# Kernel tuning notes

Measured on AMD Instinct MI355X. Metric: run time of the kernel, lower is better.

Reference implementation:

```python
import jax, jax.numpy as jnp
import numpy as np

T, B, H, W, C = 256, 1024, 9, 9, 3
CTX, HID, ACT = 64, 256, 7

def setup_inputs() -> dict:
    key = jax.random.key(0)
    ks = jax.random.split(key, 16)
    s = 0.05
    return {
        'image': jax.random.normal(ks[0], (T, B, H, W, C), jnp.float32),
        'agent_dir': jax.random.randint(ks[1], (T, B), 0, 4, jnp.int32),
        'dones': jax.random.bernoulli(ks[2], 0.02, (T, B)),
        'context': jax.random.normal(ks[3], (B, CTX), jnp.float32),
        'c0': jnp.zeros((B, HID), jnp.float32),
        'h0': jnp.zeros((B, HID), jnp.float32),
        'conv_k': jax.random.normal(ks[4], (3, 3, C, 16), jnp.float32) * s,
        'conv_b': jnp.zeros((16,), jnp.float32),
        'emb_k': jax.random.normal(ks[5], (4, 5), jnp.float32) * s,
        'emb_b': jnp.zeros((5,), jnp.float32),
        'wi': jax.random.normal(ks[6], (784 + 5 + CTX, 4 * HID), jnp.float32) * s,
        'wh': jax.random.normal(ks[7], (HID, 4 * HID), jnp.float32) * s,
        'b_lstm': jnp.zeros((4 * HID,), jnp.float32),
        'a0_k': jax.random.normal(ks[8], (HID, 32), jnp.float32) * s,
        'a0_b': jnp.zeros((32,), jnp.float32),
        'a1_k': jax.random.normal(ks[9], (32, ACT), jnp.float32) * s,
        'a1_b': jnp.zeros((ACT,), jnp.float32),
        'cr0_k': jax.random.normal(ks[10], (HID, 32), jnp.float32) * s,
        'cr0_b': jnp.zeros((32,), jnp.float32),
        'cr1_k': jax.random.normal(ks[11], (32, 1), jnp.float32) * s,
        'cr1_b': jnp.zeros((1,), jnp.float32),
    }


def reference(image, agent_dir, dones, context, c0, h0, conv_k, conv_b,
              emb_k, emb_b, wi, wh, b_lstm, a0_k, a0_b, a1_k, a1_b,
              cr0_k, cr0_b, cr1_k, cr1_b):
    t, b = image.shape[:2]
    # Conv(16, 3x3, VALID) over flattened (T*B) batch, NHWC
    x = image.reshape(t * b, *image.shape[2:])
    img = jax.lax.conv_general_dilated(
        x, conv_k, window_strides=(1, 1), padding='VALID',
        dimension_numbers=('NHWC', 'HWIO', 'NHWC')) + conv_b
    img = jax.nn.relu(img.reshape(t, b, -1))  # (T, B, 784)
    # direction embedding: one_hot(4) -> Dense(5)
    dir_e = jax.nn.one_hot(agent_dir, 4, dtype=img.dtype) @ emb_k + emb_b
    # context broadcast over time
    ctx = jnp.broadcast_to(context[None], (t, b, context.shape[-1]))
    emb = jnp.concatenate([img, dir_e, ctx], axis=-1)  # (T, B, 853)
    # precompute input-side LSTM gates (big batched GEMM outside the scan)
    xg = emb @ wi + b_lstm  # (T, B, 4*HID)

    def step(carry, inp):
        c, h = carry
        xg_t, done = inp
        mask = done[:, None]
        c = jnp.where(mask, c0, c)  # reset carry at episode boundaries
        h = jnp.where(mask, h0, h)
        gates = xg_t + h @ wh
        i, f, g, o = jnp.split(gates, 4, axis=-1)  # flax order: i, f, g, o
        new_c = jax.nn.sigmoid(f) * c + jax.nn.sigmoid(i) * jnp.tanh(g)
        new_h = jax.nn.sigmoid(o) * jnp.tanh(new_c)
        return (new_c, new_h), new_h

    (c_fin, h_fin), ys = jax.lax.scan(step, (c0, h0), (xg, dones))
    actor = jax.nn.relu(ys @ a0_k + a0_b)
    logits = actor @ a1_k + a1_b  # Categorical logits
    critic = jax.nn.relu(ys @ cr0_k + cr0_b)
    value = jnp.squeeze(critic @ cr1_k + cr1_b, axis=-1)
    return c_fin, h_fin, logits, value
```

## Files before the change

### kernel.cpp

```cpp
#include <hip/hip_runtime.h>
#include <hip/hip_fp8.h>

typedef __bf16 bf16;
typedef __bf16 bf16x8 __attribute__((ext_vector_type(8)));
typedef __bf16 bf16x4 __attribute__((ext_vector_type(4)));
typedef float  f32x4  __attribute__((ext_vector_type(4)));

#define T_DIM 256
#define B_DIM 1024
#define HID   256
#define G4    1024
#define KIMG  784
#define KPAD  800
#define KEXT  864
#define CTXD  64
#define MROWS (T_DIM*B_DIM)
#define WPITCH 264

__device__ __forceinline__ void gll16(const void* g, void* l) {
  __builtin_amdgcn_global_load_lds((const __attribute__((address_space(1))) void*)g,
                                   (__attribute__((address_space(3))) void*)l, 16, 0, 0);
}
__device__ __forceinline__ float sigm(float x) { return 1.f / (1.f + __expf(-x)); }
__device__ __forceinline__ float tanh_(float x) {
  x = fminf(fmaxf(x, -15.f), 15.f);
  float e = __expf(2.f * x);
  return (e - 1.f) / (e + 1.f);
}
__device__ __forceinline__ void bar_lds() {
  asm volatile("s_waitcnt lgkmcnt(0)\n\ts_barrier" ::: "memory");
}
__device__ __forceinline__ unsigned char to_fp8(float f) {
  __hip_fp8_e4m3 v(f);
  return *reinterpret_cast<unsigned char*>(&v);
}

__global__ void k_wiT(const float* __restrict__ wi, bf16* __restrict__ wiT) {
  int n = blockIdx.x;
  for (int k = threadIdx.x; k < KEXT; k += 256) {
    float v = 0.f;
    if (k < KIMG) v = wi[(long)k * G4 + n];
    else if (k >= 800) v = wi[(long)(k - 11) * G4 + n];
    wiT[(long)n * KEXT + k] = (bf16)v;
  }
}
__global__ void k_ext(const float* __restrict__ ctx, bf16* __restrict__ ext) {
  int idx = blockIdx.x * 256 + threadIdx.x;
  ext[idx] = (bf16)ctx[idx];
}
__global__ void k_wh8(const float* __restrict__ wh, unsigned char* __restrict__ wh8) {
  int n = blockIdx.x;
  int k = threadIdx.x;
#pragma unroll
  for (int g = 0; g < 4; ++g)
    wh8[g * 65536 + n * 256 + k] = to_fp8(wh[k * G4 + g * 256 + n]);
}
__global__ void k_W0T(const float* __restrict__ a0k, const float* __restrict__ cr0k,
                      bf16* __restrict__ w0t) {
  int n = blockIdx.x;
  int k = threadIdx.x;
  float v = (n < 32) ? a0k[k * 32 + n] : cr0k[k * 32 + (n - 32)];
  w0t[n * HID + k] = (bf16)v;
}
__global__ void k_dirgate(const float* __restrict__ wi, const float* __restrict__ emb_k,
                          const float* __restrict__ emb_b, const float* __restrict__ b_lstm,
                          float* __restrict__ dir_gate) {
  int d = blockIdx.x;
  for (int n = threadIdx.x; n < G4; n += 256) {
    float s = b_lstm[n];
#pragma unroll
    for (int j = 0; j < 5; ++j) s += (emb_k[d * 5 + j] + emb_b[j]) * wi[(KIMG + j) * G4 + n];
    dir_gate[d * G4 + n] = s;
  }
}

#define CONV_ROWS 8
__global__ void k_conv(const float* __restrict__ img, const float* __restrict__ ck,
                       const float* __restrict__ cb, bf16* __restrict__ out) {
  __shared__ float s_img[CONV_ROWS * 243];
  __shared__ float s_k[432];
  __shared__ float s_b[16];
  long r0 = (long)blockIdx.x * CONV_ROWS;
  const float* src = img + r0 * 243;
  for (int i = threadIdx.x; i < CONV_ROWS * 243; i += 256) s_img[i] = src[i];
  for (int i = threadIdx.x; i < 432; i += 256) s_k[i] = ck[i];
  if (threadIdx.x < 16) s_b[threadIdx.x] = cb[threadIdx.x];
  __syncthreads();
  for (int idx = threadIdx.x; idx < CONV_ROWS * KPAD; idx += 256) {
    int r = idx / KPAD, c = idx % KPAD;
    float v = 0.f;
    if (c < KIMG) {
      int pix = c >> 4, ch = c & 15;
      int oy = pix / 7, ox = pix % 7;
      const float* ib = s_img + r * 243 + (oy * 9 + ox) * 3;
      v = s_b[ch];
#pragma unroll
      for (int ky = 0; ky < 3; ++ky)
#pragma unroll
        for (int kx = 0; kx < 3; ++kx)
#pragma unroll
          for (int cc = 0; cc < 3; ++cc)
            v += ib[(ky * 9 + kx) * 3 + cc] * s_k[((ky * 3 + kx) * 3 + cc) * 16 + ch];
      v = fmaxf(v, 0.f);
    }
    out[r0 * KPAD + idx] = (bf16)v;
  }
}

__global__ __launch_bounds__(256, 2)
void k_gemm_xg(const bf16* __restrict__ A, const bf16* __restrict__ ext,
               const bf16* __restrict__ Bt, const float* __restrict__ dir_gate,
               const int* __restrict__ agent_dir, bf16* __restrict__ xg) {
  __shared__ __align__(16) bf16 As[128 * 32];
  __shared__ __align__(16) bf16 Bs[128 * 32];
  const int bid = blockIdx.x;
  const int xcd = bid & 7, local = bid >> 3;
  const long m0 = (long)(xcd * 256 + (local >> 3)) * 128;
  const int n0 = (local & 7) * 128;
  const int tid = threadIdx.x, wave = tid >> 6, lane = tid & 63;
  const int row16 = lane & 15, k8 = (lane >> 4) * 8, rowg = (lane >> 4) * 4;
  const int wr = (wave >> 1) * 64, wc = (wave & 1) * 64;

  const bf16* a_src0 = A + (m0 + tid / 4) * KPAD + (tid % 4) * 8;
  const bf16* a_src1 = A + (m0 + 64 + tid / 4) * KPAD + (tid % 4) * 8;
  const bf16* e_src0 = ext + (long)(((m0) & 1023) + tid / 4) * CTXD + (tid % 4) * 8;
  const bf16* e_src1 = ext + (long)(((m0 + 64) & 1023) + tid / 4) * CTXD + (tid % 4) * 8;
  const bf16* b_src0 = Bt + (long)(n0 + tid / 4) * KEXT + (tid % 4) * 8;
  const bf16* b_src1 = Bt + (long)(n0 + 64 + tid / 4) * KEXT + (tid % 4) * 8;
  bf16* asd0 = As + wave * 512;
  bf16* asd1 = As + 2048 + wave * 512;
  bf16* bsd0 = Bs + wave * 512;
  bf16* bsd1 = Bs + 2048 + wave * 512;

  f32x4 acc[4][4];
  const f32x4 zero = {0.f, 0.f, 0.f, 0.f};
#pragma unroll
  for (int i = 0; i < 4; ++i)
#pragma unroll
    for (int j = 0; j < 4; ++j) acc[i][j] = zero;

  for (int ks = 0; ks < 27; ++ks) {
    if (ks < 25) {
      const int ko = ks * 32;
      gll16(a_src0 + ko, asd0);
      gll16(a_src1 + ko, asd1);
    } else {
      const int ko = (ks - 25) * 32;
      gll16(e_src0 + ko, asd0);
      gll16(e_src1 + ko, asd1);
    }
    const int kb = ks * 32;
    gll16(b_src0 + kb, bsd0);
    gll16(b_src1 + kb, bsd1);
    __syncthreads();
    bf16x8 af[4], bfr[4];
#pragma unroll
    for (int i = 0; i < 4; ++i)
      af[i] = *(const bf16x8*)(As + (wr + 16 * i + row16) * 32 + k8);
#pragma unroll
    for (int j = 0; j < 4; ++j)
      bfr[j] = *(const bf16x8*)(Bs + (wc + 16 * j + row16) * 32 + k8);
#pragma unroll
    for (int i = 0; i < 4; ++i)
#pragma unroll
      for (int j = 0; j < 4; ++j)
        acc[i][j] = __builtin_amdgcn_mfma_f32_16x16x32_bf16(af[i], bfr[j], acc[i][j], 0, 0, 0);
    __syncthreads();
  }
#pragma unroll
  for (int i = 0; i < 4; ++i)
#pragma unroll
    for (int j = 0; j < 4; ++j)
#pragma unroll
      for (int r = 0; r < 4; ++r) {
        long row = m0 + wr + 16 * i + rowg + r;
        int colj = n0 + wc + 16 * j + row16;
        int dv = agent_dir[row];
        float base = dir_gate[dv * G4 + colj];
        int u = colj & 255, g = colj >> 8;
        xg[row * G4 + u * 4 + g] = (bf16)(acc[i][j][r] + base);
      }
}

__global__ __launch_bounds__(1024)
void k_lstm(const bf16* __restrict__ xg, const unsigned char* __restrict__ wh8,
            const int* __restrict__ dones,
            const float* __restrict__ c0, const float* __restrict__ h0,
            bf16* __restrict__ ys, float* __restrict__ cfin, float* __restrict__ hfin) {
  __shared__ __align__(16) unsigned char wi8_lds[256 * WPITCH];
  __shared__ __align__(16) unsigned char wg8_lds[256 * WPITCH];
  __shared__ __align__(16) unsigned char h8_lds[16 * WPITCH];
  const int tid = threadIdx.x;
  const int w = tid >> 6, lane = tid & 63;
  const int col = lane & 15;
  const int kq = lane >> 4;
  const int k8 = kq * 8;
  const int rowg = kq * 4;
  const int b0 = blockIdx.x * 16;
  const int ju = 16 * w + col;

  for (int i = tid; i < 256 * 32; i += 1024) {
    int row = i >> 5, c = i & 31;
    *(long long*)(wi8_lds + row * WPITCH + c * 8) =
        *(const long long*)(wh8 + row * 256 + c * 8);
    *(long long*)(wg8_lds + row * WPITCH + c * 8) =
        *(const long long*)(wh8 + 2 * 65536 + row * 256 + c * 8);
  }
  for (int i = tid; i < 16 * HID; i += 1024) {
    int m = i >> 8, j = i & 255;
    h8_lds[m * WPITCH + j] = to_fp8(h0[(b0 + m) * HID + j]);
  }

  float creg[4], c0reg[4];
  unsigned char h0b8[4];
#pragma unroll
  for (int r = 0; r < 4; ++r) {
    float v = c0[(b0 + rowg + r) * HID + ju];
    creg[r] = v; c0reg[r] = v;
    h0b8[r] = to_fp8(h0[(b0 + rowg + r) * HID + ju]);
  }
  const unsigned char* wfp = wh8 + 1 * 65536 + ju * 256 + k8;
  const unsigned char* wop = wh8 + 3 * 65536 + ju * 256 + k8;

  int4 dnA = *(const int4*)(dones + b0 + rowg);
  bf16x4 xc[4];
  {
    const bf16* xb = xg + (long)(b0 + rowg) * G4 + ju * 4;
#pragma unroll
    for (int r = 0; r < 4; ++r)
      xc[r] = *(const bf16x4*)(xb + (long)r * G4);
  }
  long long bf_cur, bf_nxt, bo_cur, bo_nxt;
  bf_cur = *(const long long*)(wfp);
  bo_cur = *(const long long*)(wop);
  __syncthreads();

#pragma unroll 1
  for (int t = 0; t < T_DIM; ++t) {
    const int tn = (t + 1 < T_DIM) ? t + 1 : (T_DIM - 1);
    f32x4 acc[4];
    const f32x4 zero = {0.f, 0.f, 0.f, 0.f};
#pragma unroll
    for (int g = 0; g < 4; ++g) acc[g] = zero;

    int4 dnB;
#pragma unroll
    for (int ks = 0; ks < 8; ++ks) {
      {
        const int kn = (ks + 1) & 7;
        bf_nxt = *(const long long*)(wfp + kn * 32);
        bo_nxt = *(const long long*)(wop + kn * 32);
      }
      long long a8 = *(const long long*)(h8_lds + col * WPITCH + ks * 32 + k8);
      long long bi8 = *(const long long*)(wi8_lds + ju * WPITCH + ks * 32 + k8);
      long long bg8 = *(const long long*)(wg8_lds + ju * WPITCH + ks * 32 + k8);
      acc[0] = __builtin_amdgcn_mfma_f32_16x16x32_fp8_fp8(a8, bi8, acc[0], 0, 0, 0);
      acc[1] = __builtin_amdgcn_mfma_f32_16x16x32_fp8_fp8(a8, bf_cur, acc[1], 0, 0, 0);
      acc[2] = __builtin_amdgcn_mfma_f32_16x16x32_fp8_fp8(a8, bg8, acc[2], 0, 0, 0);
      acc[3] = __builtin_amdgcn_mfma_f32_16x16x32_fp8_fp8(a8, bo_cur, acc[3], 0, 0, 0);
      bf_cur = bf_nxt; bo_cur = bo_nxt;
      if (ks == 2)
        dnB = *(const int4*)(dones + (long)tn * B_DIM + b0 + rowg);
    }
    bar_lds();

    int dc[4] = {dnA.x, dnA.y, dnA.z, dnA.w};
    int dx[4] = {dnB.x, dnB.y, dnB.z, dnB.w};
#pragma unroll
    for (int r = 0; r < 4; ++r) {
      float c_old = dc[r] ? c0reg[r] : creg[r];
      float gi = acc[0][r] + (float)xc[r][0];
      float gf = acc[1][r] + (float)xc[r][1];
      float gg = acc[2][r] + (float)xc[r][2];
      float go = acc[3][r] + (float)xc[r][3];
      float cn = sigm(gf) * c_old + sigm(gi) * tanh_(gg);
      float hn = sigm(go) * tanh_(cn);
      creg[r] = cn;
      int m = rowg + r;
      ys[((long)t * B_DIM + b0 + m) * HID + ju] = (bf16)hn;
      h8_lds[m * WPITCH + ju] = dx[r] ? h0b8[r] : to_fp8(hn);
      if (t == T_DIM - 1) {
        cfin[(b0 + m) * HID + ju] = cn;
        hfin[(b0 + m) * HID + ju] = hn;
      }
    }
    {
      const bf16* xb = xg + (long)(tn * B_DIM + b0 + rowg) * G4 + ju * 4;
#pragma unroll
      for (int r = 0; r < 4; ++r)
        xc[r] = *(const bf16x4*)(xb + (long)r * G4);
    }
    dnA = dnB;
    bar_lds();
  }
}

#define H1PITCH 66
__global__ __launch_bounds__(256, 2)
void k_heads(const bf16* __restrict__ ys, const bf16* __restrict__ w0t,
             const float* __restrict__ a0b, const float* __restrict__ cr0b,
             const float* __restrict__ a1k, const float* __restrict__ a1b,
             const float* __restrict__ cr1k, const float* __restrict__ cr1b,
             float* __restrict__ logits, float* __restrict__ value) {
  __shared__ __align__(16) bf16 As[128 * 32];
  __shared__ __align__(16) bf16 Ws[64 * 264];
  __shared__ bf16 h1_lds[128 * H1PITCH];
  __shared__ float w2[32 * 8];
  const int tid = threadIdx.x, wave = tid >> 6, lane = tid & 63;
  const int row16 = lane & 15, k8 = (lane >> 4) * 8, rowg = (lane >> 4) * 4;
  const long m0 = (long)blockIdx.x * 128;
  for (int i = tid; i < 64 * 256; i += 256) {
    int n = i >> 8, k = i & 255;
    Ws[n * 264 + k] = w0t[i];
  }
  if (tid < 224) { int k = tid / 7, c = tid % 7; w2[k * 8 + c] = a1k[tid]; }
  else if (tid < 256) { int k = tid - 224; w2[k * 8 + 7] = cr1k[k]; }
  const bf16* a_src0 = ys + (m0 + tid / 4) * HID + (tid % 4) * 8;
  const bf16* a_src1 = ys + (m0 + 64 + tid / 4) * HID + (tid % 4) * 8;
  bf16* asd0 = As + wave * 512;
  bf16* asd1 = As + 2048 + wave * 512;
  f32x4 acc[2][4];
  const f32x4 zero = {0.f, 0.f, 0.f, 0.f};
#pragma unroll
  for (int i = 0; i < 2; ++i)
#pragma unroll
    for (int j = 0; j < 4; ++j) acc[i][j] = zero;
  for (int ks = 0; ks < 8; ++ks) {
    gll16(a_src0 + ks * 32, asd0);
    gll16(a_src1 + ks * 32, asd1);
    __syncthreads();
    bf16x8 bw[4];
#pragma unroll
    for (int j = 0; j < 4; ++j)
      bw[j] = *(const bf16x8*)(Ws + (16 * j + row16) * 264 + ks * 32 + k8);
#pragma unroll
    for (int i = 0; i < 2; ++i) {
      bf16x8 a = *(const bf16x8*)(As + (32 * wave + 16 * i + row16) * 32 + k8);
#pragma unroll
      for (int j = 0; j < 4; ++j)
        acc[i][j] = __builtin_amdgcn_mfma_f32_16x16x32_bf16(a, bw[j], acc[i][j], 0, 0, 0);
    }
    __syncthreads();
  }
#pragma unroll
  for (int i = 0; i < 2; ++i)
#pragma unroll
    for (int j = 0; j < 4; ++j)
#pragma unroll
      for (int r = 0; r < 4; ++r) {
        int rl = 32 * wave + 16 * i + rowg + r;
        int n = 16 * j + row16;
        float bias = (n < 32) ? a0b[n] : cr0b[n - 32];
        h1_lds[rl * H1PITCH + n] = (bf16)fmaxf(acc[i][j][r] + bias, 0.f);
      }
  __syncthreads();
  if (tid < 128) {
    const bf16* hp = h1_lds + tid * H1PITCH;
    float acc7[7];
#pragma unroll
    for (int c = 0; c < 7; ++c) acc7[c] = a1b[c];
    float accv = cr1b[0];
#pragma unroll 4
    for (int k = 0; k < 32; ++k) {
      float av = (float)hp[k];
      float cv = (float)hp[32 + k];
#pragma unroll
      for (int c = 0; c < 7; ++c) acc7[c] += av * w2[k * 8 + c];
      accv += cv * w2[k * 8 + 7];
    }
    long row = m0 + tid;
#pragma unroll
    for (int c = 0; c < 7; ++c) logits[row * 7 + c] = acc7[c];
    value[row] = accv;
  }
}

extern "C" void kernel_launch(void* const* d_in, const int* in_sizes, int n_in,
                              void* d_out, int out_size, void* d_ws, size_t ws_size,
                              hipStream_t stream) {
  const float* image = (const float*)d_in[0];
  const int* agent_dir = (const int*)d_in[1];
  const int* dones = (const int*)d_in[2];
  const float* context = (const float*)d_in[3];
  const float* c0 = (const float*)d_in[4];
  const float* h0 = (const float*)d_in[5];
  const float* conv_k = (const float*)d_in[6];
  const float* conv_b = (const float*)d_in[7];
  const float* emb_k = (const float*)d_in[8];
  const float* emb_b = (const float*)d_in[9];
  const float* wi = (const float*)d_in[10];
  const float* wh = (const float*)d_in[11];
  const float* b_lstm = (const float*)d_in[12];
  const float* a0_k = (const float*)d_in[13];
  const float* a0_b = (const float*)d_in[14];
  const float* a1_k = (const float*)d_in[15];
  const float* a1_b = (const float*)d_in[16];
  const float* cr0_k = (const float*)d_in[17];
  const float* cr0_b = (const float*)d_in[18];
  const float* cr1_k = (const float*)d_in[19];
  const float* cr1_b = (const float*)d_in[20];

  char* ws = (char*)d_ws;
  const size_t off_conv = 0;
  const size_t off_xg   = 419430400ULL;
  const size_t off_wiT  = off_xg  + 536870912ULL;
  const size_t off_W0T  = off_wiT + 1769472ULL;
  const size_t off_dirg = off_W0T + 32768ULL;
  const size_t off_wh8  = off_dirg + 16384ULL;
  const size_t off_ext  = off_wh8 + 262144ULL;
  const size_t total    = off_ext + 131072ULL;
  if (ws_size < total) return;

  bf16* conv_out = (bf16*)(ws + off_conv);
  bf16* xg       = (bf16*)(ws + off_xg);
  bf16* wiT      = (bf16*)(ws + off_wiT);
  bf16* W0T      = (bf16*)(ws + off_W0T);
  float* dir_gate = (float*)(ws + off_dirg);
  unsigned char* wh8 = (unsigned char*)(ws + off_wh8);
  bf16* ext = (bf16*)(ws + off_ext);
  bf16* ys = (bf16*)(ws + 0);

  float* out_cfin = (float*)d_out;
  float* out_hfin = out_cfin + 262144;
  float* out_logits = out_cfin + 524288;
  float* out_value = out_cfin + 524288 + 1835008;

  k_wiT<<<1024, 256, 0, stream>>>(wi, wiT);
  k_ext<<<256, 256, 0, stream>>>(context, ext);
  k_W0T<<<64, 256, 0, stream>>>(a0_k, cr0_k, W0T);
  k_dirgate<<<4, 256, 0, stream>>>(wi, emb_k, emb_b, b_lstm, dir_gate);
  k_wh8<<<256, 256, 0, stream>>>(wh, wh8);
  k_conv<<<MROWS / CONV_ROWS, 256, 0, stream>>>(image, conv_k, conv_b, conv_out);
  k_gemm_xg<<<16384, 256, 0, stream>>>(conv_out, ext, wiT, dir_gate, agent_dir, xg);
  k_lstm<<<64, 1024, 0, stream>>>(xg, wh8, dones, c0, h0, ys, out_cfin, out_hfin);
  k_heads<<<2048, 256, 0, stream>>>(ys, W0T, a0_b, cr0_b, a1_k, a1_b, cr1_k, cr1_b,
                                    out_logits, out_value);
}
```

Baseline: 2.429 ms.

## Double-buffer LSTM hidden state in LDS and compute conv per pixel

The LSTM recurrence kernel now ping-pongs the fp8 hidden-state buffer between two LDS slots, so one of the two block-wide barriers per timestep can be removed. The conv kernel is also restructured so each thread computes all 16 output channels for one pixel, reusing each input load across channels and writing with vectorized bf16x8 stores. A separate pass zeroes the padded columns. Costs are slightly more LDS and higher register use in the conv kernel.

```diff
diff --git a/kernel.cpp b/kernel.cpp
--- a/kernel.cpp
+++ b/kernel.cpp
@@ -86,24 +86,37 @@
   for (int i = threadIdx.x; i < 432; i += 256) s_k[i] = ck[i];
   if (threadIdx.x < 16) s_b[threadIdx.x] = cb[threadIdx.x];
   __syncthreads();
-  for (int idx = threadIdx.x; idx < CONV_ROWS * KPAD; idx += 256) {
-    int r = idx / KPAD, c = idx % KPAD;
-    float v = 0.f;
-    if (c < KIMG) {
-      int pix = c >> 4, ch = c & 15;
-      int oy = pix / 7, ox = pix % 7;
-      const float* ib = s_img + r * 243 + (oy * 9 + ox) * 3;
-      v = s_b[ch];
-#pragma unroll
-      for (int ky = 0; ky < 3; ++ky)
-#pragma unroll
-        for (int kx = 0; kx < 3; ++kx)
-#pragma unroll
-          for (int cc = 0; cc < 3; ++cc)
-            v += ib[(ky * 9 + kx) * 3 + cc] * s_k[((ky * 3 + kx) * 3 + cc) * 16 + ch];
-      v = fmaxf(v, 0.f);
-    }
-    out[r0 * KPAD + idx] = (bf16)v;
+  if (threadIdx.x < 128) {
+    int r = threadIdx.x >> 4, c = 784 + (threadIdx.x & 15);
+    out[(r0 + r) * KPAD + c] = (bf16)0.f;
+  }
+  for (int pi = threadIdx.x; pi < CONV_ROWS * 49; pi += 256) {
+    int r = pi / 49, p = pi - r * 49;
+    int oy = p / 7, ox = p - oy * 7;
+    const float* ib = s_img + r * 243 + (oy * 9 + ox) * 3;
+    float acc[16];
+#pragma unroll
+    for (int ch = 0; ch < 16; ++ch) acc[ch] = s_b[ch];
+#pragma unroll
+    for (int ky = 0; ky < 3; ++ky)
+#pragma unroll
+      for (int kx = 0; kx < 3; ++kx)
+#pragma unroll
+        for (int cc = 0; cc < 3; ++cc) {
+          float iv = ib[(ky * 9 + kx) * 3 + cc];
+          const float* kp = s_k + ((ky * 3 + kx) * 3 + cc) * 16;
+#pragma unroll
+          for (int ch = 0; ch < 16; ++ch) acc[ch] += iv * kp[ch];
+        }
+    bf16x8 v0, v1;
+#pragma unroll
+    for (int ch = 0; ch < 8; ++ch) {
+      v0[ch] = (bf16)fmaxf(acc[ch], 0.f);
+      v1[ch] = (bf16)fmaxf(acc[ch + 8], 0.f);
+    }
+    bf16* op = out + (r0 + r) * KPAD + p * 16;
+    *(bf16x8*)op = v0;
+    *(bf16x8*)(op + 8) = v1;
   }
 }
 
@@ -189,7 +202,7 @@
             bf16* __restrict__ ys, float* __restrict__ cfin, float* __restrict__ hfin) {
   __shared__ __align__(16) unsigned char wi8_lds[256 * WPITCH];
   __shared__ __align__(16) unsigned char wg8_lds[256 * WPITCH];
-  __shared__ __align__(16) unsigned char h8_lds[16 * WPITCH];
+  __shared__ __align__(16) unsigned char h8_lds[2][16 * WPITCH];
   const int tid = threadIdx.x;
   const int w = tid >> 6, lane = tid & 63;
   const int col = lane & 15;
@@ -208,7 +221,7 @@
   }
   for (int i = tid; i < 16 * HID; i += 1024) {
     int m = i >> 8, j = i & 255;
-    h8_lds[m * WPITCH + j] = to_fp8(h0[(b0 + m) * HID + j]);
+    h8_lds[0][m * WPITCH + j] = to_fp8(h0[(b0 + m) * HID + j]);
   }
 
   float creg[4], c0reg[4];
@@ -234,6 +247,9 @@
   bf_cur = *(const long long*)(wfp);
   bo_cur = *(const long long*)(wop);
   __syncthreads();
+
+  const unsigned char* hr = h8_lds[0];
+  unsigned char* hw = (unsigned char*)h8_lds[1];
 
 #pragma unroll 1
   for (int t = 0; t < T_DIM; ++t) {
@@ -251,7 +267,7 @@
         bf_nxt = *(const long long*)(wfp + kn * 32);
         bo_nxt = *(const long long*)(wop + kn * 32);
       }
-      long long a8 = *(const long long*)(h8_lds + col * WPITCH + ks * 32 + k8);
+      long long a8 = *(const long long*)(hr + col * WPITCH + ks * 32 + k8);
       long long bi8 = *(const long long*)(wi8_lds + ju * WPITCH + ks * 32 + k8);
       long long bg8 = *(const long long*)(wg8_lds + ju * WPITCH + ks * 32 + k8);
       acc[0] = __builtin_amdgcn_mfma_f32_16x16x32_fp8_fp8(a8, bi8, acc[0], 0, 0, 0);
@@ -262,7 +278,6 @@
       if (ks == 2)
         dnB = *(const int4*)(dones + (long)tn * B_DIM + b0 + rowg);
     }
-    bar_lds();
 
     int dc[4] = {dnA.x, dnA.y, dnA.z, dnA.w};
     int dx[4] = {dnB.x, dnB.y, dnB.z, dnB.w};
@@ -278,7 +293,7 @@
       creg[r] = cn;
       int m = rowg + r;
       ys[((long)t * B_DIM + b0 + m) * HID + ju] = (bf16)hn;
-      h8_lds[m * WPITCH + ju] = dx[r] ? h0b8[r] : to_fp8(hn);
+      hw[m * WPITCH + ju] = dx[r] ? h0b8[r] : to_fp8(hn);
       if (t == T_DIM - 1) {
         cfin[(b0 + m) * HID + ju] = cn;
         hfin[(b0 + m) * HID + ju] = hn;
@@ -292,6 +307,7 @@
     }
     dnA = dnB;
     bar_lds();
+    { const unsigned char* tmp = hr; hr = hw; hw = (unsigned char*)tmp; }
   }
 }
 
```

After: 5.591 ms. 2.3x slower.
